# Kernel tuning notes

Hardware: AMD Instinct MI355X
Metric: run time of the kernel (lower is better)

## Reference

```python
import jax, jax.numpy as jnp
import numpy as np

T = 1048576          # number of time steps in the trace
SIGMA_NUM = 8
EPSILON_NUM = 8
FEAT = 2 + SIGMA_NUM + EPSILON_NUM  # [t, r_obs, sigmas..., epsilons...]


def setup_inputs() -> dict:
    key = jax.random.key(0)
    ks = jax.random.split(key, 6)
    trace = jax.random.normal(ks[0], (T, FEAT), dtype=jnp.float32)
    # column 0 is time: sorted grid with small dt so the 1M-step recurrence stays bounded
    trace = trace.at[:, 0].set(jnp.arange(T, dtype=jnp.float32) * 1e-3)
    # column 1 row 0 is the initial rate; keep it positive-ish
    trace = trace.at[0, 1].set(0.05)
    sigma_W = jax.random.normal(ks[1], (1, SIGMA_NUM), dtype=jnp.float32) * 0.01
    sigma_b = jax.random.normal(ks[2], (1,), dtype=jnp.float32) * 0.01
    eps_W = jax.random.normal(ks[3], (1, EPSILON_NUM), dtype=jnp.float32) * 0.01
    k = jnp.abs(jax.random.normal(ks[4], (1,), dtype=jnp.float32)) * 0.1
    theta = jnp.abs(jax.random.normal(ks[5], (1,), dtype=jnp.float32)) * 0.05
    return {"trace_data": trace, "sigma_W": sigma_W, "sigma_b": sigma_b,
            "eps_W": eps_W, "k": k, "theta": theta}


def reference(trace_data, sigma_W, sigma_b, eps_W, k, theta):
    S, E = SIGMA_NUM, EPSILON_NUM
    t = trace_data[:, 0]
    dts = t[1:] - t[:-1]                                   # [T-1]
    # sigma/epsilon projections depend only on trace data -> vectorize outside scan
    sig = trace_data[:-1, 2:2 + S] @ sigma_W[0] + sigma_b[0]   # [T-1]
    eps = trace_data[:-1, 2 + S:2 + S + E] @ eps_W[0]          # [T-1]
    kk = k[0]
    th = theta[0]
    r0 = trace_data[0, 1]

    def step(r, x):
        dt, s, e = x
        ode = r + kk * (th - r) * dt
        sde = s * jnp.sqrt(jnp.abs(r * dt)) * e
        r_next = ode + sde
        return r_next, r_next

    _, r_predicts = jax.lax.scan(step, r0, (dts, sig, eps))   # [T-1]
    regs = 2.0 * kk * th - sig ** 2                           # [T-1]
    return r_predicts, regs, dts
```

## Files before the change

### kernel.cpp

```cpp
#include <hip/hip_runtime.h>
#include <math.h>

#define NSTEPS  1048575
#define NPAD    1048576
#define FEAT    18
#define CLEN    4
#define CHUNKS  (NPAD / CLEN)
#define K2B     256
#define K2T     1024

__global__ void prep_kernel(const float* __restrict__ trace,
                            const float* __restrict__ sW, const float* __restrict__ sb,
                            const float* __restrict__ eW, const float* __restrict__ kp,
                            const float* __restrict__ thp,
                            float2* __restrict__ dc, float* __restrict__ seeds,
                            float* __restrict__ out, unsigned int* __restrict__ cnt)
{
    int n = blockIdx.x * blockDim.x + threadIdx.x;
    if (n == 0) *cnt = 0;
    if (n >= NSTEPS) { dc[n] = make_float2(0.f, 0.f); return; }
    const float2* r2 = (const float2*)(trace + (long)n * FEAT);
    float2 e0 = r2[0], e1 = r2[1], e2 = r2[2], e3 = r2[3], e4 = r2[4];
    float2 e5 = r2[5], e6 = r2[6], e7 = r2[7], e8 = r2[8];
    float tn1 = trace[(long)(n + 1) * FEAT];
    float d = tn1 - e0.x;
    float sig = sb[0];
    sig = fmaf(e1.x, sW[0], sig); sig = fmaf(e1.y, sW[1], sig);
    sig = fmaf(e2.x, sW[2], sig); sig = fmaf(e2.y, sW[3], sig);
    sig = fmaf(e3.x, sW[4], sig); sig = fmaf(e3.y, sW[5], sig);
    sig = fmaf(e4.x, sW[6], sig); sig = fmaf(e4.y, sW[7], sig);
    float ep = 0.f;
    ep = fmaf(e5.x, eW[0], ep); ep = fmaf(e5.y, eW[1], ep);
    ep = fmaf(e6.x, eW[2], ep); ep = fmaf(e6.y, eW[3], ep);
    ep = fmaf(e7.x, eW[4], ep); ep = fmaf(e7.y, eW[5], ep);
    ep = fmaf(e8.x, eW[6], ep); ep = fmaf(e8.y, eW[7], ep);
    float k = kp[0], th = thp[0];
    dc[n] = make_float2(d, sig * ep * sqrtf(fabsf(d)));
    out[NSTEPS + n]     = fmaf(-sig, sig, 2.f * k * th);
    out[2 * NSTEPS + n] = d;
    if ((n & 3) == 0)
        seeds[n >> 2] = th + (trace[1] - th) * __expf(-k * (e0.x - trace[0]));
}

#define GSTEP(dd, cc) { \
    float a   = fmaf(-k, (dd), 1.f); \
    float b   = kth * (dd); \
    float ar  = fabsf(r); \
    float sq  = sqrtf(ar); \
    float inv = (ar > 1e-30f) ? rsqrtf(ar) : 0.f; \
    float g   = fmaf(0.5f * (cc), copysignf(inv, r), a); \
    r = fmaf((cc), sq, fmaf(a, r, b)); \
    P *= g; }

#define FSTEP(dd, cc) { \
    float a = fmaf(-k, (dd), 1.f); \
    float b = kth * (dd); \
    rr = fmaf((cc), sqrtf(fabsf(rr)), fmaf(a, rr, b)); }

__device__ __forceinline__ void wave_scan_affine(float& A, float& B, int lane) {
#pragma unroll
    for (int d = 1; d < 64; d <<= 1) {
        float pA = __shfl_up(A, d, 64);
        float pB = __shfl_up(B, d, 64);
        if (lane >= d) { B = fmaf(A, pB, B); A *= pA; }
    }
}

__global__ void __launch_bounds__(K2T) fused_pass(
    const float2* __restrict__ dc, const float* __restrict__ seeds,
    const float* __restrict__ trace,
    const float* __restrict__ kp, const float* __restrict__ thp,
    float* __restrict__ out,
    float* __restrict__ gA, float* __restrict__ gB,
    unsigned int* __restrict__ cnt)
{
    __shared__ float wAs[16], wBs[16];
    __shared__ float sgA[K2B], sgB[K2B];
    const int tid = threadIdx.x, lane = tid & 63, wid = tid >> 6, bid = blockIdx.x;
    const int c = bid * K2T + tid;
    const float k = kp[0], th = thp[0], kth = k * th;
    const float4 q0 = ((const float4*)dc)[2 * c];
    const float4 q1 = ((const float4*)dc)[2 * c + 1];
    const float s = seeds[c];

    float r = s, P = 1.f;
    GSTEP(q0.x, q0.y)
    GSTEP(q0.z, q0.w)
    GSTEP(q1.x, q1.y)
    GSTEP(q1.z, q1.w)
    float A = P, B = fmaf(-P, s, r);

    float iA = A, iB = B;
    wave_scan_affine(iA, iB, lane);
    if (lane == 63) { wAs[wid] = iA; wBs[wid] = iB; }
    __syncthreads();
    if (wid == 0) {
        float aA = (lane < 16) ? wAs[lane] : 1.f;
        float aB = (lane < 16) ? wBs[lane] : 0.f;
        wave_scan_affine(aA, aB, lane);
        if (lane < 16) { wAs[lane] = aA; wBs[lane] = aB; }
    }
    __syncthreads();
    float weA = 1.f, weB = 0.f;
    if (wid > 0) { weA = wAs[wid - 1]; weB = wBs[wid - 1]; }
    float eA = __shfl_up(iA, 1, 64), eB = __shfl_up(iB, 1, 64);
    if (lane == 0) { eA = 1.f; eB = 0.f; }
    float Ate = eA * weA;
    float Bte = fmaf(eA, weB, eB);

    if (tid == 0) {
        __hip_atomic_store(&gA[bid], wAs[15], __ATOMIC_RELAXED, __HIP_MEMORY_SCOPE_AGENT);
        __hip_atomic_store(&gB[bid], wBs[15], __ATOMIC_RELAXED, __HIP_MEMORY_SCOPE_AGENT);
        __hip_atomic_fetch_add(cnt, 1u, __ATOMIC_ACQ_REL, __HIP_MEMORY_SCOPE_AGENT);
        while (__hip_atomic_load(cnt, __ATOMIC_ACQUIRE, __HIP_MEMORY_SCOPE_AGENT) < K2B)
            __builtin_amdgcn_s_sleep(1);
    }
    __syncthreads();

    if (tid < K2B) {
        sgA[tid] = __hip_atomic_load(&gA[tid], __ATOMIC_RELAXED, __HIP_MEMORY_SCOPE_AGENT);
        sgB[tid] = __hip_atomic_load(&gB[tid], __ATOMIC_RELAXED, __HIP_MEMORY_SCOPE_AGENT);
    }
    __syncthreads();
    for (int d = 1; d < K2B; d <<= 1) {
        float pA = 1.f, pB = 0.f;
        bool act = (tid < K2B) && (tid >= d);
        if (act) { pA = sgA[tid - d]; pB = sgB[tid - d]; }
        __syncthreads();
        if (act) { sgB[tid] = fmaf(sgA[tid], pB, sgB[tid]); sgA[tid] *= pA; }
        __syncthreads();
    }
    float beA = 1.f, beB = 0.f;
    if (bid > 0) { beA = sgA[bid - 1]; beB = sgB[bid - 1]; }

    float FA = Ate * beA;
    float FB = fmaf(Ate, beB, Bte);
    float rr = fmaf(FA, trace[1], FB);
    float4 ov;
    FSTEP(q0.x, q0.y) ov.x = rr;
    FSTEP(q0.z, q0.w) ov.y = rr;
    FSTEP(q1.x, q1.y) ov.z = rr;
    FSTEP(q1.z, q1.w) ov.w = rr;
    int nb = 4 * c;
    if (nb + 4 <= NSTEPS) {
        *(float4*)(out + nb) = ov;
    } else {
        out[nb + 0] = ov.x;
        out[nb + 1] = ov.y;
        out[nb + 2] = ov.z;
    }
}

extern "C" void kernel_launch(void* const* d_in, const int* in_sizes, int n_in,
                              void* d_out, int out_size, void* d_ws, size_t ws_size,
                              hipStream_t stream)
{
    const float* trace = (const float*)d_in[0];
    const float* sW    = (const float*)d_in[1];
    const float* sb    = (const float*)d_in[2];
    const float* eW    = (const float*)d_in[3];
    const float* kp    = (const float*)d_in[4];
    const float* thp   = (const float*)d_in[5];
    float* out = (float*)d_out;

    float*        w     = (float*)d_ws;
    float2*       dc    = (float2*)w;
    float*        seeds = w + 2 * NPAD;
    float*        gA    = seeds + CHUNKS;
    float*        gB    = gA + K2B;
    unsigned int* cnt   = (unsigned int*)(gB + K2B);

    prep_kernel<<<NPAD / 256, 256, 0, stream>>>(trace, sW, sb, eW, kp, thp,
                                                dc, seeds, out, cnt);
    fused_pass<<<K2B, K2T, 0, stream>>>(dc, seeds, trace, kp, thp, out, gA, gB, cnt);
}
```

Before: 128.7 us.

## Fuse prep kernel into single-pass scan kernel with persistent ticket barrier

Folds the projection and dt computation into the scan kernel, so each thread loads its four trace rows (72 floats) directly and computes d, coefficient and outputs in registers. The intermediate dc/seeds workspace round trip and the second kernel launch go away. The grid barrier now uses a monotonically increasing device-global ticket instead of a counter reset by a prior kernel. The cost is heavier register use (a 72-float array per thread at 1024 threads per block) and uncoalesced strided row loads inside the latency-critical kernel.

```diff
diff --git a/kernel.cpp b/kernel.cpp
--- a/kernel.cpp
+++ b/kernel.cpp
@@ -2,45 +2,13 @@
 #include <math.h>
 
 #define NSTEPS  1048575
-#define NPAD    1048576
 #define FEAT    18
-#define CLEN    4
-#define CHUNKS  (NPAD / CLEN)
-#define K2B     256
-#define K2T     1024
+#define NT      1024
+#define NB      256
+#define CHUNKS  (NT * NB)
 
-__global__ void prep_kernel(const float* __restrict__ trace,
-                            const float* __restrict__ sW, const float* __restrict__ sb,
-                            const float* __restrict__ eW, const float* __restrict__ kp,
-                            const float* __restrict__ thp,
-                            float2* __restrict__ dc, float* __restrict__ seeds,
-                            float* __restrict__ out, unsigned int* __restrict__ cnt)
-{
-    int n = blockIdx.x * blockDim.x + threadIdx.x;
-    if (n == 0) *cnt = 0;
-    if (n >= NSTEPS) { dc[n] = make_float2(0.f, 0.f); return; }
-    const float2* r2 = (const float2*)(trace + (long)n * FEAT);
-    float2 e0 = r2[0], e1 = r2[1], e2 = r2[2], e3 = r2[3], e4 = r2[4];
-    float2 e5 = r2[5], e6 = r2[6], e7 = r2[7], e8 = r2[8];
-    float tn1 = trace[(long)(n + 1) * FEAT];
-    float d = tn1 - e0.x;
-    float sig = sb[0];
-    sig = fmaf(e1.x, sW[0], sig); sig = fmaf(e1.y, sW[1], sig);
-    sig = fmaf(e2.x, sW[2], sig); sig = fmaf(e2.y, sW[3], sig);
-    sig = fmaf(e3.x, sW[4], sig); sig = fmaf(e3.y, sW[5], sig);
-    sig = fmaf(e4.x, sW[6], sig); sig = fmaf(e4.y, sW[7], sig);
-    float ep = 0.f;
-    ep = fmaf(e5.x, eW[0], ep); ep = fmaf(e5.y, eW[1], ep);
-    ep = fmaf(e6.x, eW[2], ep); ep = fmaf(e6.y, eW[3], ep);
-    ep = fmaf(e7.x, eW[4], ep); ep = fmaf(e7.y, eW[5], ep);
-    ep = fmaf(e8.x, eW[6], ep); ep = fmaf(e8.y, eW[7], ep);
-    float k = kp[0], th = thp[0];
-    dc[n] = make_float2(d, sig * ep * sqrtf(fabsf(d)));
-    out[NSTEPS + n]     = fmaf(-sig, sig, 2.f * k * th);
-    out[2 * NSTEPS + n] = d;
-    if ((n & 3) == 0)
-        seeds[n >> 2] = th + (trace[1] - th) * __expf(-k * (e0.x - trace[0]));
-}
+__device__ unsigned int g_ticket = 0;
+__device__ float gAb[NB], gBb[NB];
 
 #define GSTEP(dd, cc) { \
     float a   = fmaf(-k, (dd), 1.f); \
@@ -66,28 +34,60 @@
     }
 }
 
-__global__ void __launch_bounds__(K2T) fused_pass(
-    const float2* __restrict__ dc, const float* __restrict__ seeds,
+__global__ void __launch_bounds__(NT) cir_one(
     const float* __restrict__ trace,
-    const float* __restrict__ kp, const float* __restrict__ thp,
-    float* __restrict__ out,
-    float* __restrict__ gA, float* __restrict__ gB,
-    unsigned int* __restrict__ cnt)
+    const float* __restrict__ sW, const float* __restrict__ sb,
+    const float* __restrict__ eW, const float* __restrict__ kp,
+    const float* __restrict__ thp,
+    float* __restrict__ out)
 {
     __shared__ float wAs[16], wBs[16];
-    __shared__ float sgA[K2B], sgB[K2B];
+    __shared__ float sgA[NB], sgB[NB];
     const int tid = threadIdx.x, lane = tid & 63, wid = tid >> 6, bid = blockIdx.x;
-    const int c = bid * K2T + tid;
+    const int c = bid * NT + tid;
+    const bool lastc = (c == CHUNKS - 1);
+
     const float k = kp[0], th = thp[0], kth = k * th;
-    const float4 q0 = ((const float4*)dc)[2 * c];
-    const float4 q1 = ((const float4*)dc)[2 * c + 1];
-    const float s = seeds[c];
+    const float sbv = sb[0];
+    float sWv[8], eWv[8];
+#pragma unroll
+    for (int j = 0; j < 8; ++j) { sWv[j] = sW[j]; eWv[j] = eW[j]; }
 
+    float L[72];
+    const float4* tp = (const float4*)(trace + 72l * c);
+#pragma unroll
+    for (int i = 0; i < 18; ++i) ((float4*)L)[i] = tp[i];
+    float t4 = lastc ? L[54] : trace[72l * (c + 1)];
+
+    float dv[4], cv[4];
+#pragma unroll
+    for (int i = 0; i < 4; ++i) {
+        int base = 18 * i;
+        float tn1 = (i < 3) ? L[base + 18] : t4;
+        float d = tn1 - L[base];
+        float sig = sbv;
+#pragma unroll
+        for (int j = 0; j < 8; ++j) sig = fmaf(L[base + 2 + j], sWv[j], sig);
+        float ep = 0.f;
+#pragma unroll
+        for (int j = 0; j < 8; ++j) ep = fmaf(L[base + 10 + j], eWv[j], ep);
+        bool valid = (i < 3) || !lastc;
+        dv[i] = valid ? d : 0.f;
+        cv[i] = valid ? sig * ep * sqrtf(fabsf(d)) : 0.f;
+        if (valid) {
+            int n = 4 * c + i;
+            out[NSTEPS + n]     = fmaf(-sig, sig, 2.f * k * th);
+            out[2 * NSTEPS + n] = d;
+        }
+    }
+
+    const float r0 = trace[1];
+    const float s = th + (r0 - th) * __expf(-k * (L[0] - trace[0]));
     float r = s, P = 1.f;
-    GSTEP(q0.x, q0.y)
-    GSTEP(q0.z, q0.w)
-    GSTEP(q1.x, q1.y)
-    GSTEP(q1.z, q1.w)
+    GSTEP(dv[0], cv[0])
+    GSTEP(dv[1], cv[1])
+    GSTEP(dv[2], cv[2])
+    GSTEP(dv[3], cv[3])
     float A = P, B = fmaf(-P, s, r);
 
     float iA = A, iB = B;
@@ -109,22 +109,24 @@
     float Bte = fmaf(eA, weB, eB);
 
     if (tid == 0) {
-        __hip_atomic_store(&gA[bid], wAs[15], __ATOMIC_RELAXED, __HIP_MEMORY_SCOPE_AGENT);
-        __hip_atomic_store(&gB[bid], wBs[15], __ATOMIC_RELAXED, __HIP_MEMORY_SCOPE_AGENT);
-        __hip_atomic_fetch_add(cnt, 1u, __ATOMIC_ACQ_REL, __HIP_MEMORY_SCOPE_AGENT);
-        while (__hip_atomic_load(cnt, __ATOMIC_ACQUIRE, __HIP_MEMORY_SCOPE_AGENT) < K2B)
+        __hip_atomic_store(&gAb[bid], wAs[15], __ATOMIC_RELAXED, __HIP_MEMORY_SCOPE_AGENT);
+        __hip_atomic_store(&gBb[bid], wBs[15], __ATOMIC_RELAXED, __HIP_MEMORY_SCOPE_AGENT);
+        unsigned int tk = __hip_atomic_fetch_add(&g_ticket, 1u, __ATOMIC_ACQ_REL,
+                                                 __HIP_MEMORY_SCOPE_AGENT);
+        unsigned int target = (tk / NB + 1u) * NB;
+        while (__hip_atomic_load(&g_ticket, __ATOMIC_ACQUIRE, __HIP_MEMORY_SCOPE_AGENT) < target)
             __builtin_amdgcn_s_sleep(1);
     }
     __syncthreads();
 
-    if (tid < K2B) {
-        sgA[tid] = __hip_atomic_load(&gA[tid], __ATOMIC_RELAXED, __HIP_MEMORY_SCOPE_AGENT);
-        sgB[tid] = __hip_atomic_load(&gB[tid], __ATOMIC_RELAXED, __HIP_MEMORY_SCOPE_AGENT);
+    if (tid < NB) {
+        sgA[tid] = __hip_atomic_load(&gAb[tid], __ATOMIC_RELAXED, __HIP_MEMORY_SCOPE_AGENT);
+        sgB[tid] = __hip_atomic_load(&gBb[tid], __ATOMIC_RELAXED, __HIP_MEMORY_SCOPE_AGENT);
     }
     __syncthreads();
-    for (int d = 1; d < K2B; d <<= 1) {
+    for (int d = 1; d < NB; d <<= 1) {
         float pA = 1.f, pB = 0.f;
-        bool act = (tid < K2B) && (tid >= d);
+        bool act = (tid < NB) && (tid >= d);
         if (act) { pA = sgA[tid - d]; pB = sgB[tid - d]; }
         __syncthreads();
         if (act) { sgB[tid] = fmaf(sgA[tid], pB, sgB[tid]); sgA[tid] *= pA; }
@@ -135,14 +137,14 @@
 
     float FA = Ate * beA;
     float FB = fmaf(Ate, beB, Bte);
-    float rr = fmaf(FA, trace[1], FB);
+    float rr = fmaf(FA, r0, FB);
     float4 ov;
-    FSTEP(q0.x, q0.y) ov.x = rr;
-    FSTEP(q0.z, q0.w) ov.y = rr;
-    FSTEP(q1.x, q1.y) ov.z = rr;
-    FSTEP(q1.z, q1.w) ov.w = rr;
+    FSTEP(dv[0], cv[0]) ov.x = rr;
+    FSTEP(dv[1], cv[1]) ov.y = rr;
+    FSTEP(dv[2], cv[2]) ov.z = rr;
+    FSTEP(dv[3], cv[3]) ov.w = rr;
     int nb = 4 * c;
-    if (nb + 4 <= NSTEPS) {
+    if (!lastc) {
         *(float4*)(out + nb) = ov;
     } else {
         out[nb + 0] = ov.x;
@@ -163,14 +165,5 @@
     const float* thp   = (const float*)d_in[5];
     float* out = (float*)d_out;
 
-    float*        w     = (float*)d_ws;
-    float2*       dc    = (float2*)w;
-    float*        seeds = w + 2 * NPAD;
-    float*        gA    = seeds + CHUNKS;
-    float*        gB    = gA + K2B;
-    unsigned int* cnt   = (unsigned int*)(gB + K2B);
-
-    prep_kernel<<<NPAD / 256, 256, 0, stream>>>(trace, sW, sb, eW, kp, thp,
-                                                dc, seeds, out, cnt);
-    fused_pass<<<K2B, K2T, 0, stream>>>(dc, seeds, trace, kp, thp, out, gA, gB, cnt);
+    cir_one<<<NB, NT, 0, stream>>>(trace, sW, sb, eW, kp, thp, out);
 }
```

After: 167.9 us. +30.4%, slower.

## Process row pairs with float4 loads in prep; use persistent ticket barrier

Applied to the files above, without the earlier changes.

The prep kernel now handles two time steps per thread, so each pair of rows is read with nine aligned float4 loads. The next row's time value is fetched with a wave shuffle instead of a separate global load, and the pair's outputs are written as wider stores. The grid barrier in the scan kernel now uses a monotonically increasing device-global ticket, which removes the per-launch counter reset and the workspace barrier slots. This risks subtle ordering issues with the global ticket across launches, and halves the thread count in prep.

```diff
diff --git a/kernel.cpp b/kernel.cpp
--- a/kernel.cpp
+++ b/kernel.cpp
@@ -4,42 +4,76 @@
 #define NSTEPS  1048575
 #define NPAD    1048576
 #define FEAT    18
-#define CLEN    4
-#define CHUNKS  (NPAD / CLEN)
+#define PAIRS   (NPAD / 2)
+#define CHUNKS  (NPAD / 4)
 #define K2B     256
 #define K2T     1024
 
-__global__ void prep_kernel(const float* __restrict__ trace,
-                            const float* __restrict__ sW, const float* __restrict__ sb,
-                            const float* __restrict__ eW, const float* __restrict__ kp,
-                            const float* __restrict__ thp,
-                            float2* __restrict__ dc, float* __restrict__ seeds,
-                            float* __restrict__ out, unsigned int* __restrict__ cnt)
+__device__ unsigned int g_ticket = 0;
+__device__ float gAb[K2B], gBb[K2B];
+
+__global__ void __launch_bounds__(256) prep_kernel(
+    const float* __restrict__ trace,
+    const float* __restrict__ sW, const float* __restrict__ sb,
+    const float* __restrict__ eW, const float* __restrict__ kp,
+    const float* __restrict__ thp,
+    float2* __restrict__ dc, float* __restrict__ seeds,
+    float* __restrict__ out)
 {
-    int n = blockIdx.x * blockDim.x + threadIdx.x;
-    if (n == 0) *cnt = 0;
-    if (n >= NSTEPS) { dc[n] = make_float2(0.f, 0.f); return; }
-    const float2* r2 = (const float2*)(trace + (long)n * FEAT);
-    float2 e0 = r2[0], e1 = r2[1], e2 = r2[2], e3 = r2[3], e4 = r2[4];
-    float2 e5 = r2[5], e6 = r2[6], e7 = r2[7], e8 = r2[8];
-    float tn1 = trace[(long)(n + 1) * FEAT];
-    float d = tn1 - e0.x;
-    float sig = sb[0];
-    sig = fmaf(e1.x, sW[0], sig); sig = fmaf(e1.y, sW[1], sig);
-    sig = fmaf(e2.x, sW[2], sig); sig = fmaf(e2.y, sW[3], sig);
-    sig = fmaf(e3.x, sW[4], sig); sig = fmaf(e3.y, sW[5], sig);
-    sig = fmaf(e4.x, sW[6], sig); sig = fmaf(e4.y, sW[7], sig);
-    float ep = 0.f;
-    ep = fmaf(e5.x, eW[0], ep); ep = fmaf(e5.y, eW[1], ep);
-    ep = fmaf(e6.x, eW[2], ep); ep = fmaf(e6.y, eW[3], ep);
-    ep = fmaf(e7.x, eW[4], ep); ep = fmaf(e7.y, eW[5], ep);
-    ep = fmaf(e8.x, eW[6], ep); ep = fmaf(e8.y, eW[7], ep);
-    float k = kp[0], th = thp[0];
-    dc[n] = make_float2(d, sig * ep * sqrtf(fabsf(d)));
-    out[NSTEPS + n]     = fmaf(-sig, sig, 2.f * k * th);
-    out[2 * NSTEPS + n] = d;
-    if ((n & 3) == 0)
-        seeds[n >> 2] = th + (trace[1] - th) * __expf(-k * (e0.x - trace[0]));
+    const int p = blockIdx.x * blockDim.x + threadIdx.x;
+    const int lane = threadIdx.x & 63;
+
+    const float4* q = (const float4*)(trace + 36l * p);
+    float4 R0 = q[0], R1 = q[1], R2 = q[2], R3 = q[3], R4 = q[4];
+    float4 R5 = q[5], R6 = q[6], R7 = q[7], R8 = q[8];
+
+    float nt = __shfl_down(R0.x, 1, 64);
+    if (lane == 63) nt = (p + 1 < PAIRS) ? trace[36l * (p + 1)] : 0.f;
+
+    const float k = kp[0], th = thp[0];
+    const float sbv = sb[0];
+    const bool  v1 = (p < PAIRS - 1);
+
+    float sig0 = sbv;
+    sig0 = fmaf(R0.z, sW[0], sig0); sig0 = fmaf(R0.w, sW[1], sig0);
+    sig0 = fmaf(R1.x, sW[2], sig0); sig0 = fmaf(R1.y, sW[3], sig0);
+    sig0 = fmaf(R1.z, sW[4], sig0); sig0 = fmaf(R1.w, sW[5], sig0);
+    sig0 = fmaf(R2.x, sW[6], sig0); sig0 = fmaf(R2.y, sW[7], sig0);
+    float ep0 = 0.f;
+    ep0 = fmaf(R2.z, eW[0], ep0); ep0 = fmaf(R2.w, eW[1], ep0);
+    ep0 = fmaf(R3.x, eW[2], ep0); ep0 = fmaf(R3.y, eW[3], ep0);
+    ep0 = fmaf(R3.z, eW[4], ep0); ep0 = fmaf(R3.w, eW[5], ep0);
+    ep0 = fmaf(R4.x, eW[6], ep0); ep0 = fmaf(R4.y, eW[7], ep0);
+    float d0 = R4.z - R0.x;
+
+    float sig1 = sbv;
+    sig1 = fmaf(R5.x, sW[0], sig1); sig1 = fmaf(R5.y, sW[1], sig1);
+    sig1 = fmaf(R5.z, sW[2], sig1); sig1 = fmaf(R5.w, sW[3], sig1);
+    sig1 = fmaf(R6.x, sW[4], sig1); sig1 = fmaf(R6.y, sW[5], sig1);
+    sig1 = fmaf(R6.z, sW[6], sig1); sig1 = fmaf(R6.w, sW[7], sig1);
+    float ep1 = 0.f;
+    ep1 = fmaf(R7.x, eW[0], ep1); ep1 = fmaf(R7.y, eW[1], ep1);
+    ep1 = fmaf(R7.z, eW[2], ep1); ep1 = fmaf(R7.w, eW[3], ep1);
+    ep1 = fmaf(R8.x, eW[4], ep1); ep1 = fmaf(R8.y, eW[5], ep1);
+    ep1 = fmaf(R8.z, eW[6], ep1); ep1 = fmaf(R8.w, eW[7], ep1);
+    float d1 = nt - R4.z;
+
+    float c0 = sig0 * ep0 * sqrtf(fabsf(d0));
+    float c1 = v1 ? sig1 * ep1 * sqrtf(fabsf(d1)) : 0.f;
+    ((float4*)dc)[p] = make_float4(d0, c0, v1 ? d1 : 0.f, c1);
+
+    const int n = 2 * p;
+    float kth2 = 2.f * k * th;
+    out[NSTEPS + n] = fmaf(-sig0, sig0, kth2);
+    if (v1) {
+        out[NSTEPS + n + 1] = fmaf(-sig1, sig1, kth2);
+        *(float2*)(out + 2 * NSTEPS + n) = make_float2(d0, d1);
+    } else {
+        out[2 * NSTEPS + n] = d0;
+    }
+
+    if ((p & 1) == 0)
+        seeds[p >> 1] = th + (trace[1] - th) * __expf(-k * (R0.x - trace[0]));
 }
 
 #define GSTEP(dd, cc) { \
@@ -70,9 +104,7 @@
     const float2* __restrict__ dc, const float* __restrict__ seeds,
     const float* __restrict__ trace,
     const float* __restrict__ kp, const float* __restrict__ thp,
-    float* __restrict__ out,
-    float* __restrict__ gA, float* __restrict__ gB,
-    unsigned int* __restrict__ cnt)
+    float* __restrict__ out)
 {
     __shared__ float wAs[16], wBs[16];
     __shared__ float sgA[K2B], sgB[K2B];
@@ -109,17 +141,19 @@
     float Bte = fmaf(eA, weB, eB);
 
     if (tid == 0) {
-        __hip_atomic_store(&gA[bid], wAs[15], __ATOMIC_RELAXED, __HIP_MEMORY_SCOPE_AGENT);
-        __hip_atomic_store(&gB[bid], wBs[15], __ATOMIC_RELAXED, __HIP_MEMORY_SCOPE_AGENT);
-        __hip_atomic_fetch_add(cnt, 1u, __ATOMIC_ACQ_REL, __HIP_MEMORY_SCOPE_AGENT);
-        while (__hip_atomic_load(cnt, __ATOMIC_ACQUIRE, __HIP_MEMORY_SCOPE_AGENT) < K2B)
+        __hip_atomic_store(&gAb[bid], wAs[15], __ATOMIC_RELAXED, __HIP_MEMORY_SCOPE_AGENT);
+        __hip_atomic_store(&gBb[bid], wBs[15], __ATOMIC_RELEASE, __HIP_MEMORY_SCOPE_AGENT);
+        unsigned int tk = __hip_atomic_fetch_add(&g_ticket, 1u, __ATOMIC_ACQ_REL,
+                                                 __HIP_MEMORY_SCOPE_AGENT);
+        unsigned int target = (tk / K2B + 1u) * K2B;
+        while (__hip_atomic_load(&g_ticket, __ATOMIC_ACQUIRE, __HIP_MEMORY_SCOPE_AGENT) < target)
             __builtin_amdgcn_s_sleep(1);
     }
     __syncthreads();
 
     if (tid < K2B) {
-        sgA[tid] = __hip_atomic_load(&gA[tid], __ATOMIC_RELAXED, __HIP_MEMORY_SCOPE_AGENT);
-        sgB[tid] = __hip_atomic_load(&gB[tid], __ATOMIC_RELAXED, __HIP_MEMORY_SCOPE_AGENT);
+        sgA[tid] = __hip_atomic_load(&gAb[tid], __ATOMIC_RELAXED, __HIP_MEMORY_SCOPE_AGENT);
+        sgB[tid] = __hip_atomic_load(&gBb[tid], __ATOMIC_RELAXED, __HIP_MEMORY_SCOPE_AGENT);
     }
     __syncthreads();
     for (int d = 1; d < K2B; d <<= 1) {
@@ -163,14 +197,11 @@
     const float* thp   = (const float*)d_in[5];
     float* out = (float*)d_out;
 
-    float*        w     = (float*)d_ws;
-    float2*       dc    = (float2*)w;
-    float*        seeds = w + 2 * NPAD;
-    float*        gA    = seeds + CHUNKS;
-    float*        gB    = gA + K2B;
-    unsigned int* cnt   = (unsigned int*)(gB + K2B);
-
-    prep_kernel<<<NPAD / 256, 256, 0, stream>>>(trace, sW, sb, eW, kp, thp,
-                                                dc, seeds, out, cnt);
-    fused_pass<<<K2B, K2T, 0, stream>>>(dc, seeds, trace, kp, thp, out, gA, gB, cnt);
-}
+    float*  w     = (float*)d_ws;
+    float2* dc    = (float2*)w;
+    float*  seeds = w + 2 * NPAD;
+
+    prep_kernel<<<PAIRS / 256, 256, 0, stream>>>(trace, sW, sb, eW, kp, thp,
+                                                 dc, seeds, out);
+    fused_pass<<<K2B, K2T, 0, stream>>>(dc, seeds, trace, kp, thp, out);
+}
```

After: 133.0 us. +3.3%, slower.
